# Kernel tuning notes

Measured on AMD Instinct MI355X. Metric: run time of the kernel, lower is better.

Reference implementation:

```python
import jax, jax.numpy as jnp
import numpy as np

B, L, D_MODEL = 2, 2048, 1024
EXPAND, D_CONV, N_STATE = 2, 4, 16
D_INNER = D_MODEL * EXPAND
DT_RANK = -(-D_MODEL // 16)  # ceil(d_model/16) = 64
EPS = 1e-5


def setup_inputs() -> dict:
    key = jax.random.key(0)
    ks = jax.random.split(key, 8)
    s = 0.02
    x = jax.random.normal(ks[0], (B, L, D_MODEL), dtype=jnp.float32)
    norm_w = jnp.ones((D_MODEL,), jnp.float32)
    in_proj_w = jax.random.normal(ks[1], (D_MODEL, 2 * D_INNER), jnp.float32) * s
    conv_w = jax.random.normal(ks[2], (D_INNER, D_CONV), jnp.float32) * s  # depthwise taps
    conv_b = jnp.zeros((D_INNER,), jnp.float32)
    x_proj_w = jax.random.normal(ks[3], (D_INNER, DT_RANK + 2 * N_STATE), jnp.float32) * s
    dt_proj_w = jax.random.normal(ks[4], (DT_RANK, D_INNER), jnp.float32) * s
    dt_proj_b = jax.random.normal(ks[5], (D_INNER,), jnp.float32) * s
    A_log = jnp.log(jnp.broadcast_to(jnp.arange(1, N_STATE + 1, dtype=jnp.float32), (D_INNER, N_STATE)))
    D_param = jnp.ones((D_INNER,), jnp.float32)
    out_proj_w = jax.random.normal(ks[6], (D_INNER, D_MODEL), jnp.float32) * s
    return {"x": x, "norm_w": norm_w, "in_proj_w": in_proj_w, "conv_w": conv_w,
            "conv_b": conv_b, "x_proj_w": x_proj_w, "dt_proj_w": dt_proj_w,
            "dt_proj_b": dt_proj_b, "A_log": A_log, "D_param": D_param,
            "out_proj_w": out_proj_w}


def _block(x, norm_w, in_proj_w, conv_w, conv_b, x_proj_w, dt_proj_w, dt_proj_b,
           A_log, D_param, out_proj_w):
    b, l, _ = x.shape
    # RmsNorm
    xn = x * jax.lax.rsqrt(jnp.mean(x * x, axis=-1, keepdims=True) + EPS) * norm_w
    # in_proj and split
    x_and_res = xn @ in_proj_w                      # [b,l,2*d_inner]
    u, res = jnp.split(x_and_res, 2, axis=-1)
    # causal depthwise conv1d (pad left d_conv-1, truncate to l)
    d_conv = conv_w.shape[1]
    xp = jnp.pad(u, ((0, 0), (d_conv - 1, 0), (0, 0)))
    u = sum(xp[:, k:k + l, :] * conv_w[:, k] for k in range(d_conv)) + conv_b
    u = jax.nn.silu(u)
    # SSM projections
    x_dbl = u @ x_proj_w                            # [b,l,dt_rank+2n]
    delta, Bm, Cm = jnp.split(x_dbl, [DT_RANK, DT_RANK + N_STATE], axis=-1)
    delta = jax.nn.softplus(delta @ dt_proj_w + dt_proj_b)  # [b,l,d_inner]
    A = -jnp.exp(A_log)                             # [d_inner, n]
    deltaA = jnp.exp(jnp.einsum('bld,dn->bldn', delta, A))
    deltaB_u = jnp.einsum('bld,bln->bldn', delta * u, Bm)
    # sequential selective scan over l
    def step(h, t):
        dA_t, dBu_t, C_t = t                        # [b,d,n],[b,d,n],[b,n]
        h = dA_t * h + dBu_t
        y = jnp.einsum('bdn,bn->bd', h, C_t)
        return h, y
    h0 = jnp.zeros((b, u.shape[-1], N_STATE), deltaA.dtype)
    _, ys = jax.lax.scan(step, h0, (jnp.swapaxes(deltaA, 0, 1),
                                    jnp.swapaxes(deltaB_u, 0, 1),
                                    jnp.swapaxes(Cm, 0, 1)))
    y = jnp.swapaxes(ys, 0, 1) + u * D_param        # [b,l,d_inner]
    y = y * jax.nn.silu(res)
    return y @ out_proj_w


def reference(x, norm_w, in_proj_w, conv_w, conv_b, x_proj_w, dt_proj_w,
              dt_proj_b, A_log, D_param, out_proj_w):
    return _block(x, norm_w, in_proj_w, conv_w, conv_b, x_proj_w, dt_proj_w,
                  dt_proj_b, A_log, D_param, out_proj_w)
```

## Files before the change

### kernel.cpp

```cpp
#include <hip/hip_runtime.h>
#include <hip/hip_bf16.h>
#include <math.h>

#define B_    2
#define L_    2048
#define DM    1024
#define DI    2048
#define NTOK  (B_*L_)
#define NST   16
#define DTR   64
#define XD    96
#define DCONV 4
#define EPS   1e-5f
#define CH    64
#define NCH   (L_/CH)
#define KSP   8

typedef __attribute__((ext_vector_type(8))) short bf16x8;
typedef __attribute__((ext_vector_type(4))) float f32x4;

__device__ __forceinline__ unsigned short f2bf(float f) {
    union { float f; unsigned int u; } v; v.f = f;
    unsigned int r = v.u + 0x7fffu + ((v.u >> 16) & 1u);
    return (unsigned short)(r >> 16);
}
__device__ __forceinline__ float bf2f(unsigned short h) {
    union { unsigned int u; float f; } v; v.u = ((unsigned int)h) << 16;
    return v.f;
}

__global__ __launch_bounds__(256) void rmsnorm_bf16(const float* __restrict__ x,
    const float* __restrict__ nw, unsigned short* __restrict__ xn)
{
    const int row = blockIdx.x;
    const int tid = threadIdx.x;
    const float* xr = x + (size_t)row * DM;
    float4 v = *(const float4*)(xr + tid * 4);
    float s = v.x*v.x + v.y*v.y + v.z*v.z + v.w*v.w;
    #pragma unroll
    for (int m = 1; m < 64; m <<= 1) s += __shfl_xor(s, m);
    __shared__ float wsum[4];
    if ((tid & 63) == 0) wsum[tid >> 6] = s;
    __syncthreads();
    float tot = wsum[0] + wsum[1] + wsum[2] + wsum[3];
    float rs = rsqrtf(tot * (1.0f / DM) + EPS);
    float4 w = *(const float4*)(nw + tid * 4);
    ushort4 o;
    o.x = f2bf(v.x*rs*w.x); o.y = f2bf(v.y*rs*w.y);
    o.z = f2bf(v.z*rs*w.z); o.w = f2bf(v.w*rs*w.w);
    *(ushort4*)(xn + (size_t)row * DM + tid * 4) = o;
}

__global__ __launch_bounds__(256) void transpose_cast(const float* __restrict__ W,
    unsigned short* __restrict__ Wt, int K, int N)
{
    __shared__ float tile[32][33];
    const int tid = threadIdx.x;
    const int k0 = blockIdx.y * 32;
    const int n0 = blockIdx.x * 32;
    #pragma unroll
    for (int p = 0; p < 4; ++p) {
        int idx = p * 256 + tid;
        int r = idx >> 5, c = idx & 31;
        tile[c][r] = W[(size_t)(k0 + r) * N + n0 + c];
    }
    __syncthreads();
    #pragma unroll
    for (int p = 0; p < 4; ++p) {
        int idx = p * 256 + tid;
        int r = idx >> 5, c = idx & 31;
        Wt[(size_t)(n0 + r) * K + k0 + c] = f2bf(tile[r][c]);
    }
}

__global__ __launch_bounds__(256) void transpose_cast_hl(const float* __restrict__ W,
    unsigned short* __restrict__ Wh, unsigned short* __restrict__ Wl, int K, int N)
{
    __shared__ float tile[32][33];
    const int tid = threadIdx.x;
    const int k0 = blockIdx.y * 32;
    const int n0 = blockIdx.x * 32;
    #pragma unroll
    for (int p = 0; p < 4; ++p) {
        int idx = p * 256 + tid;
        int r = idx >> 5, c = idx & 31;
        tile[c][r] = W[(size_t)(k0 + r) * N + n0 + c];
    }
    __syncthreads();
    #pragma unroll
    for (int p = 0; p < 4; ++p) {
        int idx = p * 256 + tid;
        int r = idx >> 5, c = idx & 31;
        float v = tile[r][c];
        unsigned short h = f2bf(v);
        float lo = v - bf2f(h);
        size_t o = (size_t)(n0 + r) * K + k0 + c;
        Wh[o] = h;
        Wl[o] = f2bf(lo);
    }
}

__global__ __launch_bounds__(256) void gemm_bf16t(
    const unsigned short* __restrict__ A, const unsigned short* __restrict__ Bt,
    float* __restrict__ C, int M, int N, int K)
{
    __shared__ unsigned short Al[128 * 32];
    __shared__ unsigned short Bl[128 * 32];
    const int tid  = threadIdx.x;
    const int lane = tid & 63;
    const int wid  = tid >> 6;
    const int wr = wid >> 1, wc = wid & 1;
    const int row0 = blockIdx.y * 128;
    const int col0 = blockIdx.x * 128;

    f32x4 acc[4][4];
    #pragma unroll
    for (int m = 0; m < 4; ++m)
        #pragma unroll
        for (int n = 0; n < 4; ++n)
            acc[m][n] = (f32x4){0.f, 0.f, 0.f, 0.f};

    const int srow = wid * 32 + (lane >> 2);
    const int kc   = (lane & 3) * 8;
    const unsigned short* Ab = A  + (size_t)(row0 + srow) * K + kc;
    const unsigned short* Bb = Bt + (size_t)(col0 + srow) * K + kc;
    unsigned short* AlB = &Al[wid * 32 * 32];
    unsigned short* BlB = &Bl[wid * 32 * 32];

    for (int kt = 0; kt < K; kt += 32) {
        __builtin_amdgcn_global_load_lds(
            (const __attribute__((address_space(1))) void*)(Ab + kt),
            (__attribute__((address_space(3))) void*)(AlB), 16, 0, 0);
        __builtin_amdgcn_global_load_lds(
            (const __attribute__((address_space(1))) void*)(Ab + kt + (size_t)16 * K),
            (__attribute__((address_space(3))) void*)(AlB + 16 * 32), 16, 0, 0);
        __builtin_amdgcn_global_load_lds(
            (const __attribute__((address_space(1))) void*)(Bb + kt),
            (__attribute__((address_space(3))) void*)(BlB), 16, 0, 0);
        __builtin_amdgcn_global_load_lds(
            (const __attribute__((address_space(1))) void*)(Bb + kt + (size_t)16 * K),
            (__attribute__((address_space(3))) void*)(BlB + 16 * 32), 16, 0, 0);
        __syncthreads();

        const int fr = lane & 15, kg = (lane >> 4) * 8;
        bf16x8 a[4], b[4];
        #pragma unroll
        for (int m = 0; m < 4; ++m)
            a[m] = *(const bf16x8*)&Al[(wr * 64 + m * 16 + fr) * 32 + kg];
        #pragma unroll
        for (int n = 0; n < 4; ++n)
            b[n] = *(const bf16x8*)&Bl[(wc * 64 + n * 16 + fr) * 32 + kg];
        #pragma unroll
        for (int m = 0; m < 4; ++m)
            #pragma unroll
            for (int n = 0; n < 4; ++n)
                acc[m][n] = __builtin_amdgcn_mfma_f32_16x16x32_bf16(a[m], b[n], acc[m][n], 0, 0, 0);
        __syncthreads();
    }

    const int fr = lane & 15, rq = lane >> 4;
    #pragma unroll
    for (int m = 0; m < 4; ++m) {
        int r0 = row0 + wr * 64 + m * 16 + rq * 4;
        #pragma unroll
        for (int n = 0; n < 4; ++n) {
            int cc = col0 + wc * 64 + n * 16 + fr;
            #pragma unroll
            for (int r = 0; r < 4; ++r)
                C[(size_t)(r0 + r) * N + cc] = acc[m][n][r];
        }
    }
}

__global__ __launch_bounds__(256) void conv_silu_kernel(const float* __restrict__ xz,
    const float* __restrict__ cw, const float* __restrict__ cb,
    float* __restrict__ uc, unsigned short* __restrict__ uh, unsigned short* __restrict__ ul)
{
    int idx = blockIdx.x * 256 + threadIdx.x;
    int d = idx & (DI - 1);
    int t = idx >> 11;
    int l = t & (L_ - 1);
    int b = t >> 11;
    float acc = cb[d];
    #pragma unroll
    for (int k = 0; k < DCONV; ++k) {
        int lp = l + k - (DCONV - 1);
        if (lp >= 0)
            acc = fmaf(xz[((size_t)(b * L_ + lp) << 12) + d], cw[d * DCONV + k], acc);
    }
    float s = acc / (1.0f + expf(-acc));
    uc[idx] = s;
    unsigned short h = f2bf(s);
    uh[idx] = h;
    ul[idx] = f2bf(s - bf2f(h));
}

__global__ __launch_bounds__(64) void xproj_mfma(
    const unsigned short* __restrict__ uh, const unsigned short* __restrict__ ul,
    const unsigned short* __restrict__ Wh, const unsigned short* __restrict__ Wl,
    float* __restrict__ part)
{
    const int lane = threadIdx.x;
    const int bid = blockIdx.x;
    const int ks = bid & (KSP - 1);
    const int mb = bid >> 3;
    const int row0 = mb * 16;
    const int k0 = ks * (DI / KSP);
    const int fr = lane & 15, kg = (lane >> 4) * 8;

    f32x4 acc[6];
    #pragma unroll
    for (int j = 0; j < 6; ++j) acc[j] = (f32x4){0.f, 0.f, 0.f, 0.f};

    for (int kk = 0; kk < DI / KSP; kk += 32) {
        const size_t abase = (size_t)(row0 + fr) * DI + k0 + kk + kg;
        bf16x8 ah = *(const bf16x8*)&uh[abase];
        bf16x8 al = *(const bf16x8*)&ul[abase];
        #pragma unroll
        for (int j = 0; j < 6; ++j) {
            const size_t bbase = (size_t)(j * 16 + fr) * DI + k0 + kk + kg;
            bf16x8 bh = *(const bf16x8*)&Wh[bbase];
            bf16x8 bl = *(const bf16x8*)&Wl[bbase];
            acc[j] = __builtin_amdgcn_mfma_f32_16x16x32_bf16(ah, bh, acc[j], 0, 0, 0);
            acc[j] = __builtin_amdgcn_mfma_f32_16x16x32_bf16(al, bh, acc[j], 0, 0, 0);
            acc[j] = __builtin_amdgcn_mfma_f32_16x16x32_bf16(ah, bl, acc[j], 0, 0, 0);
        }
    }
    const int rq = lane >> 4;
    #pragma unroll
    for (int j = 0; j < 6; ++j) {
        int col = j * 16 + fr;
        #pragma unroll
        for (int r = 0; r < 4; ++r) {
            int row = row0 + rq * 4 + r;
            part[((size_t)ks * NTOK + row) * XD + col] = acc[j][r];
        }
    }
}

__global__ __launch_bounds__(256) void xproj_reduce(const float* __restrict__ part,
    float* __restrict__ xdbl, unsigned short* __restrict__ dxh, unsigned short* __restrict__ dxl)
{
    int i = blockIdx.x * 256 + threadIdx.x;
    float s = 0.f;
    #pragma unroll
    for (int ks = 0; ks < KSP; ++ks)
        s += part[(size_t)ks * ((size_t)NTOK * XD) + i];
    xdbl[i] = s;
    int row = i / XD;
    int col = i - row * XD;
    if (col < DTR) {
        unsigned short h = f2bf(s);
        size_t o = (size_t)row * DTR + col;
        dxh[o] = h;
        dxl[o] = f2bf(s - bf2f(h));
    }
}

__global__ __launch_bounds__(64) void dtproj_mfma(
    const unsigned short* __restrict__ dxh, const unsigned short* __restrict__ dxl,
    const unsigned short* __restrict__ Wh, const unsigned short* __restrict__ Wl,
    const float* __restrict__ dtb, float* __restrict__ dt)
{
    const int lane = threadIdx.x;
    const int bid = blockIdx.x;
    const int nb = bid & 15;
    const int mb = bid >> 4;
    const int row0 = mb * 16;
    const int col0 = nb * 128;
    const int fr = lane & 15, kg = (lane >> 4) * 8;

    f32x4 acc[8];
    #pragma unroll
    for (int j = 0; j < 8; ++j) acc[j] = (f32x4){0.f, 0.f, 0.f, 0.f};

    #pragma unroll
    for (int kk = 0; kk < DTR; kk += 32) {
        const size_t abase = (size_t)(row0 + fr) * DTR + kk + kg;
        bf16x8 ah = *(const bf16x8*)&dxh[abase];
        bf16x8 al = *(const bf16x8*)&dxl[abase];
        #pragma unroll
        for (int j = 0; j < 8; ++j) {
            const size_t bbase = (size_t)(col0 + j * 16 + fr) * DTR + kk + kg;
            bf16x8 bh = *(const bf16x8*)&Wh[bbase];
            bf16x8 bl = *(const bf16x8*)&Wl[bbase];
            acc[j] = __builtin_amdgcn_mfma_f32_16x16x32_bf16(ah, bh, acc[j], 0, 0, 0);
            acc[j] = __builtin_amdgcn_mfma_f32_16x16x32_bf16(al, bh, acc[j], 0, 0, 0);
            acc[j] = __builtin_amdgcn_mfma_f32_16x16x32_bf16(ah, bl, acc[j], 0, 0, 0);
        }
    }
    const int rq = lane >> 4;
    #pragma unroll
    for (int j = 0; j < 8; ++j) {
        int col = col0 + j * 16 + fr;
        float bias = dtb[col];
        #pragma unroll
        for (int r = 0; r < 4; ++r) {
            int row = row0 + rq * 4 + r;
            float v = acc[j][r] + bias;
            float sp = (v > 20.0f) ? v : __logf(1.0f + __expf(v));
            dt[(size_t)row * DI + col] = sp;
        }
    }
}

__global__ __launch_bounds__(256) void scan_passA(
    const float* __restrict__ dt, const float* __restrict__ uc,
    const float* __restrict__ xdbl, const float* __restrict__ A_log,
    float* __restrict__ hA, float* __restrict__ PA)
{
    const int tid = threadIdx.x;
    const int bid = blockIdx.x;
    const int dblk = bid & 15;
    const int c = (bid >> 4) & (NCH - 1);
    const int b = bid >> 9;
    const int di = tid >> 1, hf = tid & 1;
    const int d = dblk * 128 + di;
    const size_t t0 = (size_t)b * L_ + (size_t)c * CH;

    float Av[8];
    {
        const float4* ap = (const float4*)(A_log + (size_t)d * NST + hf * 8);
        float4 a0 = ap[0], a1 = ap[1];
        Av[0]=-expf(a0.x); Av[1]=-expf(a0.y); Av[2]=-expf(a0.z); Av[3]=-expf(a0.w);
        Av[4]=-expf(a1.x); Av[5]=-expf(a1.y); Av[6]=-expf(a1.z); Av[7]=-expf(a1.w);
    }
    float h[8], P[8];
    #pragma unroll
    for (int n = 0; n < 8; ++n) { h[n] = 0.f; P[n] = 1.f; }

    float dtv[4], uv[4];
    float4 Bq[2][2];
    #pragma unroll
    for (int j = 0; j < 4; ++j) {
        size_t t = t0 + j;
        dtv[j] = dt[t * DI + d];
        uv[j]  = uc[t * DI + d];
    }
    #pragma unroll
    for (int j = 0; j < 2; ++j) {
        const float4* xr = (const float4*)(xdbl + (t0 + j) * XD + DTR + hf * 8);
        Bq[j][0] = xr[0]; Bq[j][1] = xr[1];
    }

    #pragma unroll 4
    for (int l = 0; l < CH; ++l) {
        const int s2 = l & 1, s4 = l & 3;
        float dtc = dtv[s4], uvc = uv[s4];
        float bc[8];
        bc[0]=Bq[s2][0].x; bc[1]=Bq[s2][0].y; bc[2]=Bq[s2][0].z; bc[3]=Bq[s2][0].w;
        bc[4]=Bq[s2][1].x; bc[5]=Bq[s2][1].y; bc[6]=Bq[s2][1].z; bc[7]=Bq[s2][1].w;
        if (l + 4 < CH) {
            size_t t = t0 + l + 4;
            dtv[s4] = dt[t * DI + d];
            uv[s4]  = uc[t * DI + d];
        }
        if (l + 2 < CH) {
            const float4* xr = (const float4*)(xdbl + (t0 + l + 2) * XD + DTR + hf * 8);
            Bq[s2][0] = xr[0]; Bq[s2][1] = xr[1];
        }
        float dtu = dtc * uvc;
        #pragma unroll
        for (int n = 0; n < 8; ++n) {
            float dA = __expf(dtc * Av[n]);
            h[n] = fmaf(dA, h[n], dtu * bc[n]);
            P[n] *= dA;
        }
    }
    size_t obase = ((size_t)(b * NCH + c) * DI + d) * NST + hf * 8;
    float4* hp = (float4*)&hA[obase];
    hp[0] = make_float4(h[0], h[1], h[2], h[3]);
    hp[1] = make_float4(h[4], h[5], h[6], h[7]);
    float4* pp = (float4*)&PA[obase];
    pp[0] = make_float4(P[0], P[1], P[2], P[3]);
    pp[1] = make_float4(P[4], P[5], P[6], P[7]);
}

__global__ __launch_bounds__(256) void scan_passB(
    const float* __restrict__ hA, const float* __restrict__ PA,
    float* __restrict__ hin)
{
    int g = blockIdx.x * 256 + threadIdx.x;
    int b = g >> 15;
    int rest = g & 32767;
    float h = 0.f;
    for (int c = 0; c < NCH; ++c) {
        size_t idx = ((size_t)(b * NCH + c) * DI) * NST + rest;
        hin[idx] = h;
        h = fmaf(PA[idx], h, hA[idx]);
    }
}

__global__ __launch_bounds__(256) void scan_passC(
    const float* __restrict__ dt, const float* __restrict__ uc,
    const float* __restrict__ xdbl, const float* __restrict__ xz,
    const float* __restrict__ A_log, const float* __restrict__ Dp,
    const float* __restrict__ hin, unsigned short* __restrict__ yg)
{
    const int tid = threadIdx.x;
    const int bid = blockIdx.x;
    const int dblk = bid & 15;
    const int c = (bid >> 4) & (NCH - 1);
    const int b = bid >> 9;
    const int di = tid >> 1, hf = tid & 1;
    const int d = dblk * 128 + di;
    const size_t t0 = (size_t)b * L_ + (size_t)c * CH;

    float Av[8];
    {
        const float4* ap = (const float4*)(A_log + (size_t)d * NST + hf * 8);
        float4 a0 = ap[0], a1 = ap[1];
        Av[0]=-expf(a0.x); Av[1]=-expf(a0.y); Av[2]=-expf(a0.z); Av[3]=-expf(a0.w);
        Av[4]=-expf(a1.x); Av[5]=-expf(a1.y); Av[6]=-expf(a1.z); Av[7]=-expf(a1.w);
    }
    const float Dv = Dp[d];
    float h[8];
    {
        size_t ibase = ((size_t)(b * NCH + c) * DI + d) * NST + hf * 8;
        const float4* hp = (const float4*)&hin[ibase];
        float4 h0 = hp[0], h1 = hp[1];
        h[0]=h0.x; h[1]=h0.y; h[2]=h0.z; h[3]=h0.w;
        h[4]=h1.x; h[5]=h1.y; h[6]=h1.z; h[7]=h1.w;
    }

    float dtv[4], uv[4], rv[4];
    float4 Bq[2][2], Cq[2][2];
    #pragma unroll
    for (int j = 0; j < 4; ++j) {
        size_t t = t0 + j;
        dtv[j] = dt[t * DI + d];
        uv[j]  = uc[t * DI + d];
        rv[j]  = xz[(t << 12) + DI + d];
    }
    #pragma unroll
    for (int j = 0; j < 2; ++j) {
        const float4* xr = (const float4*)(xdbl + (t0 + j) * XD + DTR + hf * 8);
        Bq[j][0] = xr[0]; Bq[j][1] = xr[1];
        Cq[j][0] = xr[4]; Cq[j][1] = xr[5];
    }

    #pragma unroll 4
    for (int l = 0; l < CH; ++l) {
        const int s2 = l & 1, s4 = l & 3;
        float dtc = dtv[s4], uvc = uv[s4], rvc = rv[s4];
        float bc[8], cc[8];
        bc[0]=Bq[s2][0].x; bc[1]=Bq[s2][0].y; bc[2]=Bq[s2][0].z; bc[3]=Bq[s2][0].w;
        bc[4]=Bq[s2][1].x; bc[5]=Bq[s2][1].y; bc[6]=Bq[s2][1].z; bc[7]=Bq[s2][1].w;
        cc[0]=Cq[s2][0].x; cc[1]=Cq[s2][0].y; cc[2]=Cq[s2][0].z; cc[3]=Cq[s2][0].w;
        cc[4]=Cq[s2][1].x; cc[5]=Cq[s2][1].y; cc[6]=Cq[s2][1].z; cc[7]=Cq[s2][1].w;
        if (l + 4 < CH) {
            size_t t = t0 + l + 4;
            dtv[s4] = dt[t * DI + d];
            uv[s4]  = uc[t * DI + d];
            rv[s4]  = xz[(t << 12) + DI + d];
        }
        if (l + 2 < CH) {
            const float4* xr = (const float4*)(xdbl + (t0 + l + 2) * XD + DTR + hf * 8);
            Bq[s2][0] = xr[0]; Bq[s2][1] = xr[1];
            Cq[s2][0] = xr[4]; Cq[s2][1] = xr[5];
        }
        float dtu = dtc * uvc;
        float p = 0.f;
        #pragma unroll
        for (int n = 0; n < 8; ++n) {
            float dA = __expf(dtc * Av[n]);
            h[n] = fmaf(dA, h[n], dtu * bc[n]);
            p = fmaf(h[n], cc[n], p);
        }
        p += __shfl_xor(p, 1);
        if (hf == 0) {
            float y = fmaf(uvc, Dv, p);
            float sig = 1.0f / (1.0f + __expf(-rvc));
            yg[(t0 + l) * DI + d] = f2bf(y * rvc * sig);
        }
    }
}

extern "C" void kernel_launch(void* const* d_in, const int* in_sizes, int n_in,
                              void* d_out, int out_size, void* d_ws, size_t ws_size,
                              hipStream_t stream)
{
    const float* x    = (const float*)d_in[0];
    const float* nw   = (const float*)d_in[1];
    const float* ipw  = (const float*)d_in[2];
    const float* cw   = (const float*)d_in[3];
    const float* cb   = (const float*)d_in[4];
    const float* xpw  = (const float*)d_in[5];
    const float* dtw  = (const float*)d_in[6];
    const float* dtb  = (const float*)d_in[7];
    const float* alog = (const float*)d_in[8];
    const float* dpar = (const float*)d_in[9];
    const float* opw  = (const float*)d_in[10];
    float* out = (float*)d_out;

    char* p = (char*)d_ws;
    float* xz    = (float*)p;  p += (size_t)NTOK * 2 * DI * 4;
    float* uc    = (float*)p;  p += (size_t)NTOK * DI * 4;
    float* xdbl  = (float*)p;  p += (size_t)NTOK * XD * 4;
    float* dtbuf = (float*)p;  p += (size_t)NTOK * DI * 4;
    float* hin   = (float*)p;  p += (size_t)B_ * NCH * DI * NST * 4;
    unsigned short* yg   = (unsigned short*)p;  p += (size_t)NTOK * DI * 2;
    unsigned short* xnb  = (unsigned short*)p;  p += (size_t)NTOK * DM * 2;
    unsigned short* ipwt = (unsigned short*)p;  p += (size_t)DM * 2 * DI * 2;
    unsigned short* opwt = (unsigned short*)p;  p += (size_t)DI * DM * 2;
    unsigned short* xpwh = (unsigned short*)p;  p += (size_t)XD * DI * 2;
    unsigned short* xpwl = (unsigned short*)p;  p += (size_t)XD * DI * 2;
    unsigned short* dtwh = (unsigned short*)p;  p += (size_t)DI * DTR * 2;
    unsigned short* dtwl = (unsigned short*)p;  p += (size_t)DI * DTR * 2;
    unsigned short* dxh  = (unsigned short*)p;  p += (size_t)NTOK * DTR * 2;
    unsigned short* dxl  = (unsigned short*)p;  p += (size_t)NTOK * DTR * 2;
    float* hA = (float*)xnb;
    float* PA = (float*)ipwt;
    unsigned short* uh = (unsigned short*)dtbuf;
    unsigned short* ul = (unsigned short*)(dtbuf + (size_t)NTOK * DI / 2);
    float* part = (float*)yg;

    transpose_cast<<<dim3(2 * DI / 32, DM / 32), 256, 0, stream>>>(ipw, ipwt, DM, 2 * DI);
    transpose_cast<<<dim3(DM / 32, DI / 32), 256, 0, stream>>>(opw, opwt, DI, DM);
    transpose_cast_hl<<<dim3(XD / 32, DI / 32), 256, 0, stream>>>(xpw, xpwh, xpwl, DI, XD);
    transpose_cast_hl<<<dim3(DI / 32, DTR / 32), 256, 0, stream>>>(dtw, dtwh, dtwl, DTR, DI);

    rmsnorm_bf16<<<NTOK, 256, 0, stream>>>(x, nw, xnb);

    gemm_bf16t<<<dim3(2 * DI / 128, NTOK / 128), 256, 0, stream>>>(xnb, ipwt, xz, NTOK, 2 * DI, DM);

    conv_silu_kernel<<<NTOK * DI / 256, 256, 0, stream>>>(xz, cw, cb, uc, uh, ul);

    xproj_mfma<<<(NTOK / 16) * KSP, 64, 0, stream>>>(uh, ul, xpwh, xpwl, part);
    xproj_reduce<<<NTOK * XD / 256, 256, 0, stream>>>(part, xdbl, dxh, dxl);

    dtproj_mfma<<<(NTOK / 16) * (DI / 128), 64, 0, stream>>>(dxh, dxl, dtwh, dtwl, dtb, dtbuf);

    scan_passA<<<B_ * NCH * (DI / 128), 256, 0, stream>>>(dtbuf, uc, xdbl, alog, hA, PA);
    scan_passB<<<B_ * DI * NST / 256, 256, 0, stream>>>(hA, PA, hin);
    scan_passC<<<B_ * NCH * (DI / 128), 256, 0, stream>>>(dtbuf, uc, xdbl, xz, alog, dpar, hin, yg);

    gemm_bf16t<<<dim3(DM / 128, NTOK / 128), 256, 0, stream>>>(yg, opwt, out, NTOK, DM, DI);
}
```

Measured before the change: 419.6 us.

## Swizzle GEMM LDS layout and split scan states across four threads

The bf16 GEMM now applies an XOR swizzle to the k-chunk offset on both the global-to-LDS load and the fragment read, to cut LDS bank conflicts when MFMA operands are loaded. The scan passes A and C now assign 4 threads per channel with 4 states each, instead of 2 threads with 8 states, and launch twice as many blocks. This gives more parallelism and a shorter serial dependency chain per thread. In exchange, each dt/u/res value is loaded redundantly by 4 lanes, and pass C needs an extra shuffle for the reduction.

New measurement: 461.6 us. 1.1x slower.

```diff
diff --git a/kernel.cpp b/kernel.cpp
--- a/kernel.cpp
+++ b/kernel.cpp
@@ -121,7 +121,7 @@
             acc[m][n] = (f32x4){0.f, 0.f, 0.f, 0.f};
 
     const int srow = wid * 32 + (lane >> 2);
-    const int kc   = (lane & 3) * 8;
+    const int kc   = (((lane & 3) ^ ((lane >> 3) & 3)) * 8);
     const unsigned short* Ab = A  + (size_t)(row0 + srow) * K + kc;
     const unsigned short* Bb = Bt + (size_t)(col0 + srow) * K + kc;
     unsigned short* AlB = &Al[wid * 32 * 32];
@@ -142,7 +142,8 @@
             (__attribute__((address_space(3))) void*)(BlB + 16 * 32), 16, 0, 0);
         __syncthreads();
 
-        const int fr = lane & 15, kg = (lane >> 4) * 8;
+        const int fr = lane & 15;
+        const int kg = 8 * ((lane >> 4) ^ ((fr >> 1) & 3));
         bf16x8 a[4], b[4];
         #pragma unroll
         for (int m = 0; m < 4; ++m)
@@ -311,26 +312,24 @@
 {
     const int tid = threadIdx.x;
     const int bid = blockIdx.x;
-    const int dblk = bid & 15;
-    const int c = (bid >> 4) & (NCH - 1);
-    const int b = bid >> 9;
-    const int di = tid >> 1, hf = tid & 1;
-    const int d = dblk * 128 + di;
+    const int dblk = bid & 31;
+    const int c = (bid >> 5) & (NCH - 1);
+    const int b = bid >> 10;
+    const int di = tid >> 2, q = tid & 3;
+    const int d = dblk * 64 + di;
     const size_t t0 = (size_t)b * L_ + (size_t)c * CH;
 
-    float Av[8];
+    float Av[4];
     {
-        const float4* ap = (const float4*)(A_log + (size_t)d * NST + hf * 8);
-        float4 a0 = ap[0], a1 = ap[1];
+        float4 a0 = *(const float4*)(A_log + (size_t)d * NST + q * 4);
         Av[0]=-expf(a0.x); Av[1]=-expf(a0.y); Av[2]=-expf(a0.z); Av[3]=-expf(a0.w);
-        Av[4]=-expf(a1.x); Av[5]=-expf(a1.y); Av[6]=-expf(a1.z); Av[7]=-expf(a1.w);
-    }
-    float h[8], P[8];
-    #pragma unroll
-    for (int n = 0; n < 8; ++n) { h[n] = 0.f; P[n] = 1.f; }
+    }
+    float h[4], P[4];
+    #pragma unroll
+    for (int n = 0; n < 4; ++n) { h[n] = 0.f; P[n] = 1.f; }
 
     float dtv[4], uv[4];
-    float4 Bq[2][2];
+    float4 Bq[2];
     #pragma unroll
     for (int j = 0; j < 4; ++j) {
         size_t t = t0 + j;
@@ -338,42 +337,32 @@
         uv[j]  = uc[t * DI + d];
     }
     #pragma unroll
-    for (int j = 0; j < 2; ++j) {
-        const float4* xr = (const float4*)(xdbl + (t0 + j) * XD + DTR + hf * 8);
-        Bq[j][0] = xr[0]; Bq[j][1] = xr[1];
-    }
+    for (int j = 0; j < 2; ++j)
+        Bq[j] = *(const float4*)(xdbl + (t0 + j) * XD + DTR + q * 4);
 
     #pragma unroll 4
     for (int l = 0; l < CH; ++l) {
         const int s2 = l & 1, s4 = l & 3;
         float dtc = dtv[s4], uvc = uv[s4];
-        float bc[8];
-        bc[0]=Bq[s2][0].x; bc[1]=Bq[s2][0].y; bc[2]=Bq[s2][0].z; bc[3]=Bq[s2][0].w;
-        bc[4]=Bq[s2][1].x; bc[5]=Bq[s2][1].y; bc[6]=Bq[s2][1].z; bc[7]=Bq[s2][1].w;
+        float bc[4] = {Bq[s2].x, Bq[s2].y, Bq[s2].z, Bq[s2].w};
         if (l + 4 < CH) {
             size_t t = t0 + l + 4;
             dtv[s4] = dt[t * DI + d];
             uv[s4]  = uc[t * DI + d];
         }
-        if (l + 2 < CH) {
-            const float4* xr = (const float4*)(xdbl + (t0 + l + 2) * XD + DTR + hf * 8);
-            Bq[s2][0] = xr[0]; Bq[s2][1] = xr[1];
-        }
+        if (l + 2 < CH)
+            Bq[s2] = *(const float4*)(xdbl + (t0 + l + 2) * XD + DTR + q * 4);
         float dtu = dtc * uvc;
         #pragma unroll
-        for (int n = 0; n < 8; ++n) {
+        for (int n = 0; n < 4; ++n) {
             float dA = __expf(dtc * Av[n]);
             h[n] = fmaf(dA, h[n], dtu * bc[n]);
             P[n] *= dA;
         }
     }
-    size_t obase = ((size_t)(b * NCH + c) * DI + d) * NST + hf * 8;
-    float4* hp = (float4*)&hA[obase];
-    hp[0] = make_float4(h[0], h[1], h[2], h[3]);
-    hp[1] = make_float4(h[4], h[5], h[6], h[7]);
-    float4* pp = (float4*)&PA[obase];
-    pp[0] = make_float4(P[0], P[1], P[2], P[3]);
-    pp[1] = make_float4(P[4], P[5], P[6], P[7]);
+    size_t obase = ((size_t)(b * NCH + c) * DI + d) * NST + q * 4;
+    *(float4*)&hA[obase] = make_float4(h[0], h[1], h[2], h[3]);
+    *(float4*)&PA[obase] = make_float4(P[0], P[1], P[2], P[3]);
 }
 
 __global__ __launch_bounds__(256) void scan_passB(
@@ -399,32 +388,28 @@
 {
     const int tid = threadIdx.x;
     const int bid = blockIdx.x;
-    const int dblk = bid & 15;
-    const int c = (bid >> 4) & (NCH - 1);
-    const int b = bid >> 9;
-    const int di = tid >> 1, hf = tid & 1;
-    const int d = dblk * 128 + di;
+    const int dblk = bid & 31;
+    const int c = (bid >> 5) & (NCH - 1);
+    const int b = bid >> 10;
+    const int di = tid >> 2, q = tid & 3;
+    const int d = dblk * 64 + di;
     const size_t t0 = (size_t)b * L_ + (size_t)c * CH;
 
-    float Av[8];
+    float Av[4];
     {
-        const float4* ap = (const float4*)(A_log + (size_t)d * NST + hf * 8);
-        float4 a0 = ap[0], a1 = ap[1];
+        float4 a0 = *(const float4*)(A_log + (size_t)d * NST + q * 4);
         Av[0]=-expf(a0.x); Av[1]=-expf(a0.y); Av[2]=-expf(a0.z); Av[3]=-expf(a0.w);
-        Av[4]=-expf(a1.x); Av[5]=-expf(a1.y); Av[6]=-expf(a1.z); Av[7]=-expf(a1.w);
     }
     const float Dv = Dp[d];
-    float h[8];
+    float h[4];
     {
-        size_t ibase = ((size_t)(b * NCH + c) * DI + d) * NST + hf * 8;
-        const float4* hp = (const float4*)&hin[ibase];
-        float4 h0 = hp[0], h1 = hp[1];
+        size_t ibase = ((size_t)(b * NCH + c) * DI + d) * NST + q * 4;
+        float4 h0 = *(const float4*)&hin[ibase];
         h[0]=h0.x; h[1]=h0.y; h[2]=h0.z; h[3]=h0.w;
-        h[4]=h1.x; h[5]=h1.y; h[6]=h1.z; h[7]=h1.w;
     }
 
     float dtv[4], uv[4], rv[4];
-    float4 Bq[2][2], Cq[2][2];
+    float4 Bq[2], Cq[2];
     #pragma unroll
     for (int j = 0; j < 4; ++j) {
         size_t t = t0 + j;
@@ -434,20 +419,16 @@
     }
     #pragma unroll
     for (int j = 0; j < 2; ++j) {
-        const float4* xr = (const float4*)(xdbl + (t0 + j) * XD + DTR + hf * 8);
-        Bq[j][0] = xr[0]; Bq[j][1] = xr[1];
-        Cq[j][0] = xr[4]; Cq[j][1] = xr[5];
+        Bq[j] = *(const float4*)(xdbl + (t0 + j) * XD + DTR + q * 4);
+        Cq[j] = *(const float4*)(xdbl + (t0 + j) * XD + DTR + NST + q * 4);
     }
 
     #pragma unroll 4
     for (int l = 0; l < CH; ++l) {
         const int s2 = l & 1, s4 = l & 3;
         float dtc = dtv[s4], uvc = uv[s4], rvc = rv[s4];
-        float bc[8], cc[8];
-        bc[0]=Bq[s2][0].x; bc[1]=Bq[s2][0].y; bc[2]=Bq[s2][0].z; bc[3]=Bq[s2][0].w;
-        bc[4]=Bq[s2][1].x; bc[5]=Bq[s2][1].y; bc[6]=Bq[s2][1].z; bc[7]=Bq[s2][1].w;
-        cc[0]=Cq[s2][0].x; cc[1]=Cq[s2][0].y; cc[2]=Cq[s2][0].z; cc[3]=Cq[s2][0].w;
-        cc[4]=Cq[s2][1].x; cc[5]=Cq[s2][1].y; cc[6]=Cq[s2][1].z; cc[7]=Cq[s2][1].w;
+        float bc[4] = {Bq[s2].x, Bq[s2].y, Bq[s2].z, Bq[s2].w};
+        float cc[4] = {Cq[s2].x, Cq[s2].y, Cq[s2].z, Cq[s2].w};
         if (l + 4 < CH) {
             size_t t = t0 + l + 4;
             dtv[s4] = dt[t * DI + d];
@@ -455,20 +436,20 @@
             rv[s4]  = xz[(t << 12) + DI + d];
         }
         if (l + 2 < CH) {
-            const float4* xr = (const float4*)(xdbl + (t0 + l + 2) * XD + DTR + hf * 8);
-            Bq[s2][0] = xr[0]; Bq[s2][1] = xr[1];
-            Cq[s2][0] = xr[4]; Cq[s2][1] = xr[5];
+            Bq[s2] = *(const float4*)(xdbl + (t0 + l + 2) * XD + DTR + q * 4);
+            Cq[s2] = *(const float4*)(xdbl + (t0 + l + 2) * XD + DTR + NST + q * 4);
         }
         float dtu = dtc * uvc;
         float p = 0.f;
         #pragma unroll
-        for (int n = 0; n < 8; ++n) {
+        for (int n = 0; n < 4; ++n) {
             float dA = __expf(dtc * Av[n]);
             h[n] = fmaf(dA, h[n], dtu * bc[n]);
             p = fmaf(h[n], cc[n], p);
         }
         p += __shfl_xor(p, 1);
-        if (hf == 0) {
+        p += __shfl_xor(p, 2);
+        if (q == 0) {
             float y = fmaf(uvc, Dv, p);
             float sig = 1.0f / (1.0f + __expf(-rvc));
             yg[(t0 + l) * DI + d] = f2bf(y * rvc * sig);
@@ -531,9 +512,9 @@
 
     dtproj_mfma<<<(NTOK / 16) * (DI / 128), 64, 0, stream>>>(dxh, dxl, dtwh, dtwl, dtb, dtbuf);
 
-    scan_passA<<<B_ * NCH * (DI / 128), 256, 0, stream>>>(dtbuf, uc, xdbl, alog, hA, PA);
+    scan_passA<<<B_ * NCH * (DI / 64), 256, 0, stream>>>(dtbuf, uc, xdbl, alog, hA, PA);
     scan_passB<<<B_ * DI * NST / 256, 256, 0, stream>>>(hA, PA, hin);
-    scan_passC<<<B_ * NCH * (DI / 128), 256, 0, stream>>>(dtbuf, uc, xdbl, xz, alog, dpar, hin, yg);
+    scan_passC<<<B_ * NCH * (DI / 64), 256, 0, stream>>>(dtbuf, uc, xdbl, xz, alog, dpar, hin, yg);
 
     gemm_bf16t<<<dim3(DM / 128, NTOK / 128), 256, 0, stream>>>(yg, opwt, out, NTOK, DM, DI);
 }
```
